# Kernel tuning notes

Hardware: AMD Instinct MI355X
Metric: run time of the kernel (lower is better)

Reference implementation:

```python
import jax, jax.numpy as jnp
import numpy as np

H = 1024
NH = 16
HD = H // NH  # 64
EPS = 1e-5


def _layernorm(x, g, b):
    mu = jnp.mean(x, axis=-1, keepdims=True)
    var = jnp.mean((x - mu) ** 2, axis=-1, keepdims=True)
    return (x - mu) * jax.lax.rsqrt(var + EPS) * g + b


def _rotate_half(x):
    h = x.shape[-1] // 2
    return jnp.concatenate([-x[..., h:], x[..., :h]], axis=-1)


def _rope_tables(T, hd, dtype):
    inv_freq = 1.0 / (10000.0 ** (jnp.arange(0, hd, 2, dtype=jnp.float32) / hd))
    freqs = jnp.arange(T, dtype=jnp.float32)[:, None] * inv_freq[None, :]  # [T, hd/2]
    emb = jnp.concatenate([freqs, freqs], axis=-1)  # [T, hd]
    return jnp.cos(emb).astype(dtype), jnp.sin(emb).astype(dtype)


def setup_inputs() -> dict:
    key = jax.random.key(0)
    ks = jax.random.split(key, 12)
    B, T = 32, 512
    s = 0.02
    inp = {
        "x": jax.random.normal(ks[0], (B, T, H), dtype=jnp.float32),
        "Wq": jax.random.normal(ks[1], (H, H), dtype=jnp.float32) * s,
        "bq": jnp.zeros((H,), jnp.float32),
        "Wk": jax.random.normal(ks[2], (H, H), dtype=jnp.float32) * s,
        "bk": jnp.zeros((H,), jnp.float32),
        "Wv": jax.random.normal(ks[3], (H, H), dtype=jnp.float32) * s,
        "bv": jnp.zeros((H,), jnp.float32),
        "Wo": jax.random.normal(ks[4], (H, H), dtype=jnp.float32) * s,
        "bo": jnp.zeros((H,), jnp.float32),
        "g1": jnp.ones((H,), jnp.float32),
        "be1": jnp.zeros((H,), jnp.float32),
        "g2": jnp.ones((H,), jnp.float32),
        "be2": jnp.zeros((H,), jnp.float32),
        "W1": jax.random.normal(ks[5], (H, 4 * H), dtype=jnp.float32) * s,
        "b1": jnp.zeros((4 * H,), jnp.float32),
        "W2": jax.random.normal(ks[6], (4 * H, H), dtype=jnp.float32) * s,
        "b2": jnp.zeros((H,), jnp.float32),
    }
    return inp


def reference(x, Wq, bq, Wk, bk, Wv, bv, Wo, bo, g1, be1, g2, be2, W1, b1, W2, b2):
    B, T, Hdim = x.shape
    xn = _layernorm(x, g1, be1)
    # [B,T,H] -> [B,NH,T,HD]
    def split_heads(y):
        return y.reshape(B, T, NH, HD).transpose(0, 2, 1, 3)
    q = split_heads(xn @ Wq + bq)
    k = split_heads(xn @ Wk + bk)
    v = split_heads(xn @ Wv + bv)
    cos, sin = _rope_tables(T, HD, x.dtype)  # [T,HD]
    cos = cos[None, None]
    sin = sin[None, None]
    q = q * cos + _rotate_half(q) * sin
    k = k * cos + _rotate_half(k) * sin
    scale = jnp.sqrt(jnp.asarray(HD, x.dtype))
    scores = jnp.einsum("bhqd,bhkd->bhqk", q, k) / scale
    probs = jax.nn.softmax(scores, axis=-1)
    attn = jnp.einsum("bhqk,bhkd->bhqd", probs, v)
    attn = attn.transpose(0, 2, 1, 3).reshape(B, T, Hdim)
    x = x + (attn @ Wo + bo)
    xn2 = _layernorm(x, g2, be2)
    ffn = jax.nn.gelu(xn2 @ W1 + b1, approximate=False) @ W2 + b2
    return x + ffn
```

## Files before the change

### kernel.cpp

```cpp
#include <hip/hip_runtime.h>
#include <math.h>
#include <stdint.h>

#define B_  32
#define T_  512
#define H_  1024
#define NH_ 16
#define HD_ 64
#define FF_ 4096
#define BT_ (B_*T_)
#define CB_ 8
#define CR_ (CB_*T_)
#define NC_ (B_/CB_)
#define MB_ ((size_t)1<<20)

typedef __attribute__((ext_vector_type(8))) short bf16x8;
typedef __attribute__((ext_vector_type(4))) short s16x4;
typedef __attribute__((ext_vector_type(4))) float f32x4;

__device__ __forceinline__ float bf2f(short h){
  unsigned u = ((unsigned)(unsigned short)h) << 16;
  return __uint_as_float(u);
}
__device__ __forceinline__ short f2bf(float f){
  unsigned u = __float_as_uint(f);
  unsigned r = (u + 0x7FFFu + ((u>>16)&1u)) >> 16;
  return (short)r;
}
__device__ __forceinline__ float gelu_f(float x){
  return 0.5f * x * (1.0f + erff(x * 0.7071067811865476f));
}

typedef __attribute__((address_space(1))) const unsigned guint_t;
typedef __attribute__((address_space(3))) unsigned luint_t;
__device__ __forceinline__ void gld16(const void* g, void* l){
  __builtin_amdgcn_global_load_lds((guint_t*)(uintptr_t)g,
                                   (luint_t*)(unsigned)(uintptr_t)l, 16, 0, 0);
}

__global__ __launch_bounds__(256) void ln_bf16_kernel(const float* __restrict__ x,
    const float* __restrict__ g, const float* __restrict__ b, short* __restrict__ o)
{
  const int row = blockIdx.x;
  const int tid = threadIdx.x;
  const float4 v = ((const float4*)(x + (size_t)row*H_))[tid];
  float s  = v.x+v.y+v.z+v.w;
  float ss = v.x*v.x+v.y*v.y+v.z*v.z+v.w*v.w;
  #pragma unroll
  for(int off=32; off>0; off>>=1){
    s  += __shfl_down(s, off);
    ss += __shfl_down(ss, off);
  }
  __shared__ float rs[4], rss[4], mb[2];
  const int wave = tid>>6, lane = tid&63;
  if(lane==0){ rs[wave]=s; rss[wave]=ss; }
  __syncthreads();
  if(tid==0){
    float S  = rs[0]+rs[1]+rs[2]+rs[3];
    float SS = rss[0]+rss[1]+rss[2]+rss[3];
    float mu  = S * (1.0f/H_);
    float var = SS * (1.0f/H_) - mu*mu;
    mb[0] = mu; mb[1] = rsqrtf(var + 1e-5f);
  }
  __syncthreads();
  const float mu = mb[0], rstd = mb[1];
  const float4 gv = ((const float4*)g)[tid];
  const float4 bv = ((const float4*)b)[tid];
  s16x4 o4;
  o4[0] = f2bf((v.x-mu)*rstd*gv.x + bv.x);
  o4[1] = f2bf((v.y-mu)*rstd*gv.y + bv.y);
  o4[2] = f2bf((v.z-mu)*rstd*gv.z + bv.z);
  o4[3] = f2bf((v.w-mu)*rstd*gv.w + bv.w);
  *(s16x4*)(o + (size_t)row*H_ + tid*4) = o4;
}

__global__ void rope_table_kernel(float* __restrict__ cost, float* __restrict__ sint)
{
  const int t = blockIdx.x;
  const int i = threadIdx.x;
  const float invf = (float)pow(10000.0, -(double)i / 32.0);
  const float ang  = (float)t * invf;
  cost[t*32 + i] = (float)cos((double)ang);
  sint[t*32 + i] = (float)sin((double)ang);
}

__global__ void concat3_kernel(const float* __restrict__ a, const float* __restrict__ b,
                               const float* __restrict__ c, float* __restrict__ o)
{
  int i = blockIdx.x*256 + threadIdx.x;
  if(i >= 3*H_) return;
  o[i] = (i < H_) ? a[i] : (i < 2*H_) ? b[i-H_] : c[i-2*H_];
}

__global__ __launch_bounds__(256) void tsplit_kernel(const float* __restrict__ W,
    short* __restrict__ Wh, short* __restrict__ Wl, int K, int N)
{
  __shared__ float t[32][33];
  const int n0 = blockIdx.x*32, k0 = blockIdx.y*32;
  const int tx = threadIdx.x & 31, ty = threadIdx.x >> 5;
  #pragma unroll
  for(int i=0;i<32;i+=8) t[ty+i][tx] = W[(size_t)(k0+ty+i)*N + n0+tx];
  __syncthreads();
  #pragma unroll
  for(int i=0;i<32;i+=8){
    const float f = t[tx][ty+i];
    const short h = f2bf(f);
    const short l = f2bf(f - bf2f(h));
    const size_t o = (size_t)(n0+ty+i)*K + k0+tx;
    Wh[o] = h;  Wl[o] = l;
  }
}

template<int EPI, int OB>
__global__ __launch_bounds__(256,3) void gemm_bf2(
    const short* __restrict__ A, const short* __restrict__ Bhg,
    const short* __restrict__ Blg, const float* __restrict__ bias,
    const float* __restrict__ res, void* __restrict__ Cv,
    int M, int N, int K,
    size_t zW, size_t zC, int biasZ)
{
  __shared__ __align__(16) short Ah[2][128*32];
  __shared__ __align__(16) short Bh[2][128*32];
  __shared__ __align__(16) short Bl[2][128*32];

  const int tid = threadIdx.x;
  const int wid = tid >> 6, lane = tid & 63;
  const int z = blockIdx.z;
  const int bn0 = blockIdx.x * 128;
  const int bm0 = blockIdx.y * 128;
  const short* Bhp = Bhg + (size_t)z * zW;
  const short* Blp = Blg + (size_t)z * zW;
  const float* biasp = bias + (size_t)z * biasZ;

  const int srow0 = wid*16 + (lane>>2);
  const int scol  = (lane&3)*8;

  f32x4 acc[4][4];
  #pragma unroll
  for(int i=0;i<4;i++)
    #pragma unroll
    for(int j=0;j<4;j++) acc[i][j] = (f32x4){0.f,0.f,0.f,0.f};

#define STAGE(BUF, K0) do { \
    _Pragma("unroll") \
    for(int r=0;r<2;r++){ \
      const int rr = srow0 + r*64; \
      const int lo = (r*4+wid)*512; \
      gld16(A   + (size_t)(bm0+rr)*K + (K0) + scol, &Ah[BUF][lo]); \
      gld16(Bhp + (size_t)(bn0+rr)*K + (K0) + scol, &Bh[BUF][lo]); \
      gld16(Blp + (size_t)(bn0+rr)*K + (K0) + scol, &Bl[BUF][lo]); \
    } \
  } while(0)

  STAGE(0, 0);
  __syncthreads();

  const int wm = wid >> 1, wn = wid & 1;
  const int fr = lane & 15;
  const int kq = lane >> 4;

  const int KT = K / 32;
  int buf = 0;
  for(int kt=0; kt<KT; kt++){
    if(kt+1 < KT) STAGE(buf^1, (kt+1)*32);

    bf16x8 af[4], bfh[4], bfl[4];
    #pragma unroll
    for(int mt=0;mt<4;mt++)
      af[mt]  = *(bf16x8*)&Ah[buf][(wm*64 + mt*16 + fr)*32 + kq*8];
    #pragma unroll
    for(int nt=0;nt<4;nt++){
      bfh[nt] = *(bf16x8*)&Bh[buf][(wn*64 + nt*16 + fr)*32 + kq*8];
      bfl[nt] = *(bf16x8*)&Bl[buf][(wn*64 + nt*16 + fr)*32 + kq*8];
    }
    #pragma unroll
    for(int mt=0;mt<4;mt++)
      #pragma unroll
      for(int nt=0;nt<4;nt++){
        acc[mt][nt] = __builtin_amdgcn_mfma_f32_16x16x32_bf16(af[mt], bfh[nt], acc[mt][nt], 0,0,0);
        acc[mt][nt] = __builtin_amdgcn_mfma_f32_16x16x32_bf16(af[mt], bfl[nt], acc[mt][nt], 0,0,0);
      }
    __syncthreads();
    buf ^= 1;
  }
#undef STAGE

  #pragma unroll
  for(int nt=0;nt<4;nt++){
    const int col = bn0 + wn*64 + nt*16 + fr;
    const float bb = biasp[col];
    #pragma unroll
    for(int mt=0;mt<4;mt++){
      #pragma unroll
      for(int r=0;r<4;r++){
        const size_t row = bm0 + wm*64 + mt*16 + kq*4 + r;
        float v = acc[mt][nt][r] + bb;
        if(EPI==1) v = gelu_f(v);
        if(EPI==2) v += res[row*N + col];
        if(OB) ((short*)Cv)[(size_t)z*zC + row*N + col] = f2bf(v);
        else   ((float*)Cv)[(size_t)z*zC + row*N + col] = v;
      }
    }
  }
}

__global__ __launch_bounds__(256,4) void attn_mfma_kernel(
    const short* __restrict__ qg, const short* __restrict__ kg,
    const short* __restrict__ vg, short* __restrict__ og,
    const float* __restrict__ cost, const float* __restrict__ sint)
{
  __shared__ __align__(16) short Q_lds[64][72];
  __shared__ __align__(16) short K_lds[64][72];
  __shared__ __align__(16) short Vt[64][72];
  __shared__ __align__(16) short P_lds[64][72];

  const int qt = blockIdx.x;
  const int bh = blockIdx.y;
  const int b = bh >> 4, h = bh & 15;
  const int tid = threadIdx.x;
  const int wid = tid >> 6, lane = tid & 63;
  const size_t base = ((size_t)b*T_)*H_ + (size_t)h*HD_;

  const int srow = tid >> 2;
  const int sc8  = (tid & 3) * 8;
  const int sc16 = (tid & 3) * 16;

  {
    const int t = qt*64 + srow;
    const short* qp = qg + base + (size_t)t*H_;
    bf16x8 lo = *(const bf16x8*)(qp + sc8);
    bf16x8 hi = *(const bf16x8*)(qp + sc8 + 32);
    float cc[8], ss[8];
    *(float4*)&cc[0] = *(const float4*)(cost + t*32 + sc8);
    *(float4*)&cc[4] = *(const float4*)(cost + t*32 + sc8 + 4);
    *(float4*)&ss[0] = *(const float4*)(sint + t*32 + sc8);
    *(float4*)&ss[4] = *(const float4*)(sint + t*32 + sc8 + 4);
    short olo[8], ohi[8];
    #pragma unroll
    for(int j=0;j<8;j++){
      const float x0 = bf2f(lo[j]), x1 = bf2f(hi[j]);
      olo[j] = f2bf((x0*cc[j] - x1*ss[j])*0.125f);
      ohi[j] = f2bf((x1*cc[j] + x0*ss[j])*0.125f);
    }
    *(bf16x8*)&Q_lds[srow][sc8]    = *(bf16x8*)olo;
    *(bf16x8*)&Q_lds[srow][sc8+32] = *(bf16x8*)ohi;
  }

  const int fr = lane & 15;
  const int g  = lane >> 4;
  const int wq0 = wid * 16;

  float m_run = -1e30f, l_run = 0.f;
  f32x4 acc[4];
  #pragma unroll
  for(int i=0;i<4;i++) acc[i] = (f32x4){0.f,0.f,0.f,0.f};

  for(int kt=0; kt<T_/64; kt++){
    __syncthreads();
    {
      const int t = kt*64 + srow;
      const short* kp = kg + base + (size_t)t*H_;
      bf16x8 lo = *(const bf16x8*)(kp + sc8);
      bf16x8 hi = *(const bf16x8*)(kp + sc8 + 32);
      float cc[8], ss[8];
      *(float4*)&cc[0] = *(const float4*)(cost + t*32 + sc8);
      *(float4*)&cc[4] = *(const float4*)(cost + t*32 + sc8 + 4);
      *(float4*)&ss[0] = *(const float4*)(sint + t*32 + sc8);
      *(float4*)&ss[4] = *(const float4*)(sint + t*32 + sc8 + 4);
      short olo[8], ohi[8];
      #pragma unroll
      for(int j=0;j<8;j++){
        const float x0 = bf2f(lo[j]), x1 = bf2f(hi[j]);
        olo[j] = f2bf(x0*cc[j] - x1*ss[j]);
        ohi[j] = f2bf(x1*cc[j] + x0*ss[j]);
      }
      *(bf16x8*)&K_lds[srow][sc8]    = *(bf16x8*)olo;
      *(bf16x8*)&K_lds[srow][sc8+32] = *(bf16x8*)ohi;

      const short* vp = vg + base + (size_t)t*H_;
      bf16x8 v0 = *(const bf16x8*)(vp + sc16);
      bf16x8 v1 = *(const bf16x8*)(vp + sc16 + 8);
      #pragma unroll
      for(int j=0;j<8;j++){
        Vt[sc16+j][srow]   = v0[j];
        Vt[sc16+8+j][srow] = v1[j];
      }
    }
    __syncthreads();

    f32x4 sfr[4];
    #pragma unroll
    for(int mt=0;mt<4;mt++) sfr[mt] = (f32x4){0.f,0.f,0.f,0.f};
    #pragma unroll
    for(int kk=0;kk<2;kk++){
      const bf16x8 qf = *(bf16x8*)&Q_lds[wq0 + fr][kk*32 + g*8];
      #pragma unroll
      for(int mt=0;mt<4;mt++){
        const bf16x8 kf = *(bf16x8*)&K_lds[mt*16 + fr][kk*32 + g*8];
        sfr[mt] = __builtin_amdgcn_mfma_f32_16x16x32_bf16(kf, qf, sfr[mt], 0,0,0);
      }
    }

    float tmax = -1e30f;
    #pragma unroll
    for(int mt=0;mt<4;mt++)
      #pragma unroll
      for(int r=0;r<4;r++) tmax = fmaxf(tmax, sfr[mt][r]);
    tmax = fmaxf(tmax, __shfl_xor(tmax, 16));
    tmax = fmaxf(tmax, __shfl_xor(tmax, 32));
    const float mn = fmaxf(m_run, tmax);
    const float alpha = __expf(m_run - mn);
    m_run = mn;
    float psum = 0.f;
    short pb[4][4];
    #pragma unroll
    for(int mt=0;mt<4;mt++)
      #pragma unroll
      for(int r=0;r<4;r++){
        const short pbf = f2bf(__expf(sfr[mt][r] - mn));
        pb[mt][r] = pbf;
        psum += bf2f(pbf);
      }
    psum += __shfl_xor(psum, 16);
    psum += __shfl_xor(psum, 32);
    l_run = l_run*alpha + psum;

    #pragma unroll
    for(int mt=0;mt<4;mt++)
      *(s16x4*)&P_lds[wq0 + fr][mt*16 + g*4] = *(s16x4*)pb[mt];

    float a_r[4];
    #pragma unroll
    for(int r=0;r<4;r++) a_r[r] = __shfl(alpha, (lane & 48) | (4*g + r));
    #pragma unroll
    for(int nt=0;nt<4;nt++)
      #pragma unroll
      for(int r=0;r<4;r++) acc[nt][r] *= a_r[r];

    #pragma unroll
    for(int kk=0;kk<2;kk++){
      const bf16x8 pf = *(bf16x8*)&P_lds[wq0 + fr][kk*32 + g*8];
      #pragma unroll
      for(int nt=0;nt<4;nt++){
        const bf16x8 vf = *(bf16x8*)&Vt[nt*16 + fr][kk*32 + g*8];
        acc[nt] = __builtin_amdgcn_mfma_f32_16x16x32_bf16(pf, vf, acc[nt], 0,0,0);
      }
    }
  }

  float linv[4];
  #pragma unroll
  for(int r=0;r<4;r++) linv[r] = 1.0f / __shfl(l_run, (lane & 48) | (4*g + r));
  #pragma unroll
  for(int nt=0;nt<4;nt++){
    const int d = nt*16 + fr;
    #pragma unroll
    for(int r=0;r<4;r++){
      const int t = qt*64 + wq0 + 4*g + r;
      og[base + (size_t)t*H_ + d] = f2bf(acc[nt][r] * linv[r]);
    }
  }
}

extern "C" void kernel_launch(void* const* d_in, const int* in_sizes, int n_in,
                              void* d_out, int out_size, void* d_ws, size_t ws_size,
                              hipStream_t stream)
{
  const float* x   = (const float*)d_in[0];
  const float* Wq  = (const float*)d_in[1];
  const float* bq  = (const float*)d_in[2];
  const float* Wk  = (const float*)d_in[3];
  const float* bk  = (const float*)d_in[4];
  const float* Wv  = (const float*)d_in[5];
  const float* bv  = (const float*)d_in[6];
  const float* Wo  = (const float*)d_in[7];
  const float* bo  = (const float*)d_in[8];
  const float* g1  = (const float*)d_in[9];
  const float* be1 = (const float*)d_in[10];
  const float* g2  = (const float*)d_in[11];
  const float* be2 = (const float*)d_in[12];
  const float* W1  = (const float*)d_in[13];
  const float* b1  = (const float*)d_in[14];
  const float* W2  = (const float*)d_in[15];
  const float* b2  = (const float*)d_in[16];
  float* out = (float*)d_out;
  char*  W   = (char*)d_ws;

  short* wqkvh = (short*)(W + 0*MB_);
  short* wqkvl = (short*)(W + 6*MB_);
  short* woh   = (short*)(W + 12*MB_);
  short* wol   = (short*)(W + 14*MB_);
  short* w1h   = (short*)(W + 16*MB_);
  short* w1l   = (short*)(W + 24*MB_);
  short* w2h   = (short*)(W + 32*MB_);
  short* w2l   = (short*)(W + 40*MB_);
  short* abuf  = (short*)(W + 48*MB_);
  short* hb    = abuf;
  short* qkvc  = (short*)(W + 80*MB_);
  short* xnc   = (short*)(W + 104*MB_);
  float* cost  = (float*)(W + 112*MB_);
  float* sint  = cost + T_*32;
  float* bqkv  = sint + T_*32;

  const size_t CRH = (size_t)CR_ * H_;

  rope_table_kernel<<<T_, 32, 0, stream>>>(cost, sint);
  concat3_kernel<<<(3*H_+255)/256, 256, 0, stream>>>(bq, bk, bv, bqkv);

  tsplit_kernel<<<dim3(32,32),  256, 0, stream>>>(Wq, wqkvh,            wqkvl,            H_, H_);
  tsplit_kernel<<<dim3(32,32),  256, 0, stream>>>(Wk, wqkvh+1024*1024,  wqkvl+1024*1024,  H_, H_);
  tsplit_kernel<<<dim3(32,32),  256, 0, stream>>>(Wv, wqkvh+2*1024*1024,wqkvl+2*1024*1024,H_, H_);
  tsplit_kernel<<<dim3(32,32),  256, 0, stream>>>(Wo, woh, wol, H_, H_);
  tsplit_kernel<<<dim3(128,32), 256, 0, stream>>>(W1, w1h, w1l, H_, FF_);
  tsplit_kernel<<<dim3(32,128), 256, 0, stream>>>(W2, w2h, w2l, FF_, H_);

  for(int c=0; c<NC_; c++){
    const size_t r0 = (size_t)c * CR_;
    ln_bf16_kernel<<<CR_, 256, 0, stream>>>(x + r0*H_, g1, be1, xnc);
    gemm_bf2<0,1><<<dim3(8, CR_/128, 3), 256, 0, stream>>>(
        xnc, wqkvh, wqkvl, bqkv, nullptr, qkvc, CR_, H_, H_,
        (size_t)1024*1024, CRH, H_);
    attn_mfma_kernel<<<dim3(T_/64, CB_*NH_), 256, 0, stream>>>(
        qkvc, qkvc + CRH, qkvc + 2*CRH, abuf + r0*H_, cost, sint);
  }

  gemm_bf2<2,0><<<dim3(8, BT_/128, 1), 256, 0, stream>>>(
      abuf, woh, wol, bo, x, out, BT_, H_, H_, 0, 0, 0);

  for(int c=0; c<NC_; c++){
    const size_t r0 = (size_t)c * CR_;
    ln_bf16_kernel<<<CR_, 256, 0, stream>>>(out + r0*H_, g2, be2, xnc);
    gemm_bf2<1,1><<<dim3(FF_/128, CR_/128, 1), 256, 0, stream>>>(
        xnc, w1h, w1l, b1, nullptr, hb, CR_, FF_, H_, 0, 0, 0);
    gemm_bf2<2,0><<<dim3(H_/128, CR_/128, 1), 256, 0, stream>>>(
        hb, w2h, w2l, b2, out + r0*H_, out + r0*H_, CR_, H_, FF_, 0, 0, 0);
  }
}
```

Baseline: 1.418 ms.

## Switch GEMMs and attention from split-bf16 weights to single fp16 MFMA

Replaces the hi/lo bf16 weight split (two MFMAs per tile, three LDS buffers) with one fp16 weight copy and a single fp16 MFMA per tile. Activations, Q/K/V, softmax probabilities and attention output are now stored as fp16 instead of bf16. This halves matrix-core work and weight traffic in every GEMM, cuts LDS use, and raises the launch-bounds occupancy hint from 3 to 4. In exchange it relies on fp16's mantissa to stay within accuracy tolerance, and fp16's narrower range risks overflow on large activations.

```diff
diff --git a/kernel.cpp b/kernel.cpp
--- a/kernel.cpp
+++ b/kernel.cpp
@@ -14,19 +14,11 @@
 #define NC_ (B_/CB_)
 #define MB_ ((size_t)1<<20)
 
-typedef __attribute__((ext_vector_type(8))) short bf16x8;
-typedef __attribute__((ext_vector_type(4))) short s16x4;
+typedef _Float16 h16;
+typedef __attribute__((ext_vector_type(8))) _Float16 f16x8;
+typedef __attribute__((ext_vector_type(4))) _Float16 f16x4;
 typedef __attribute__((ext_vector_type(4))) float f32x4;
 
-__device__ __forceinline__ float bf2f(short h){
-  unsigned u = ((unsigned)(unsigned short)h) << 16;
-  return __uint_as_float(u);
-}
-__device__ __forceinline__ short f2bf(float f){
-  unsigned u = __float_as_uint(f);
-  unsigned r = (u + 0x7FFFu + ((u>>16)&1u)) >> 16;
-  return (short)r;
-}
 __device__ __forceinline__ float gelu_f(float x){
   return 0.5f * x * (1.0f + erff(x * 0.7071067811865476f));
 }
@@ -38,8 +30,8 @@
                                    (luint_t*)(unsigned)(uintptr_t)l, 16, 0, 0);
 }
 
-__global__ __launch_bounds__(256) void ln_bf16_kernel(const float* __restrict__ x,
-    const float* __restrict__ g, const float* __restrict__ b, short* __restrict__ o)
+__global__ __launch_bounds__(256) void ln_f16_kernel(const float* __restrict__ x,
+    const float* __restrict__ g, const float* __restrict__ b, h16* __restrict__ o)
 {
   const int row = blockIdx.x;
   const int tid = threadIdx.x;
@@ -66,12 +58,12 @@
   const float mu = mb[0], rstd = mb[1];
   const float4 gv = ((const float4*)g)[tid];
   const float4 bv = ((const float4*)b)[tid];
-  s16x4 o4;
-  o4[0] = f2bf((v.x-mu)*rstd*gv.x + bv.x);
-  o4[1] = f2bf((v.y-mu)*rstd*gv.y + bv.y);
-  o4[2] = f2bf((v.z-mu)*rstd*gv.z + bv.z);
-  o4[3] = f2bf((v.w-mu)*rstd*gv.w + bv.w);
-  *(s16x4*)(o + (size_t)row*H_ + tid*4) = o4;
+  f16x4 o4;
+  o4[0] = (h16)((v.x-mu)*rstd*gv.x + bv.x);
+  o4[1] = (h16)((v.y-mu)*rstd*gv.y + bv.y);
+  o4[2] = (h16)((v.z-mu)*rstd*gv.z + bv.z);
+  o4[3] = (h16)((v.w-mu)*rstd*gv.w + bv.w);
+  *(f16x4*)(o + (size_t)row*H_ + tid*4) = o4;
 }
 
 __global__ void rope_table_kernel(float* __restrict__ cost, float* __restrict__ sint)
@@ -92,8 +84,8 @@
   o[i] = (i < H_) ? a[i] : (i < 2*H_) ? b[i-H_] : c[i-2*H_];
 }
 
-__global__ __launch_bounds__(256) void tsplit_kernel(const float* __restrict__ W,
-    short* __restrict__ Wh, short* __restrict__ Wl, int K, int N)
+__global__ __launch_bounds__(256) void tcvt_kernel(const float* __restrict__ W,
+    h16* __restrict__ Wt, int K, int N)
 {
   __shared__ float t[32][33];
   const int n0 = blockIdx.x*32, k0 = blockIdx.y*32;
@@ -104,32 +96,26 @@
   #pragma unroll
   for(int i=0;i<32;i+=8){
     const float f = t[tx][ty+i];
-    const short h = f2bf(f);
-    const short l = f2bf(f - bf2f(h));
-    const size_t o = (size_t)(n0+ty+i)*K + k0+tx;
-    Wh[o] = h;  Wl[o] = l;
+    Wt[(size_t)(n0+ty+i)*K + k0+tx] = (h16)f;
   }
 }
 
 template<int EPI, int OB>
-__global__ __launch_bounds__(256,3) void gemm_bf2(
-    const short* __restrict__ A, const short* __restrict__ Bhg,
-    const short* __restrict__ Blg, const float* __restrict__ bias,
-    const float* __restrict__ res, void* __restrict__ Cv,
-    int M, int N, int K,
+__global__ __launch_bounds__(256,4) void gemm_f16(
+    const h16* __restrict__ A, const h16* __restrict__ Bg,
+    const float* __restrict__ bias, const float* __restrict__ res,
+    void* __restrict__ Cv, int M, int N, int K,
     size_t zW, size_t zC, int biasZ)
 {
-  __shared__ __align__(16) short Ah[2][128*32];
-  __shared__ __align__(16) short Bh[2][128*32];
-  __shared__ __align__(16) short Bl[2][128*32];
+  __shared__ __align__(16) h16 Ah[2][128*32];
+  __shared__ __align__(16) h16 Bh[2][128*32];
 
   const int tid = threadIdx.x;
   const int wid = tid >> 6, lane = tid & 63;
   const int z = blockIdx.z;
   const int bn0 = blockIdx.x * 128;
   const int bm0 = blockIdx.y * 128;
-  const short* Bhp = Bhg + (size_t)z * zW;
-  const short* Blp = Blg + (size_t)z * zW;
+  const h16* Bp = Bg + (size_t)z * zW;
   const float* biasp = bias + (size_t)z * biasZ;
 
   const int srow0 = wid*16 + (lane>>2);
@@ -146,9 +132,8 @@
     for(int r=0;r<2;r++){ \
       const int rr = srow0 + r*64; \
       const int lo = (r*4+wid)*512; \
-      gld16(A   + (size_t)(bm0+rr)*K + (K0) + scol, &Ah[BUF][lo]); \
-      gld16(Bhp + (size_t)(bn0+rr)*K + (K0) + scol, &Bh[BUF][lo]); \
-      gld16(Blp + (size_t)(bn0+rr)*K + (K0) + scol, &Bl[BUF][lo]); \
+      gld16(A  + (size_t)(bm0+rr)*K + (K0) + scol, &Ah[BUF][lo]); \
+      gld16(Bp + (size_t)(bn0+rr)*K + (K0) + scol, &Bh[BUF][lo]); \
     } \
   } while(0)
 
@@ -164,22 +149,18 @@
   for(int kt=0; kt<KT; kt++){
     if(kt+1 < KT) STAGE(buf^1, (kt+1)*32);
 
-    bf16x8 af[4], bfh[4], bfl[4];
+    f16x8 af[4], bf[4];
     #pragma unroll
     for(int mt=0;mt<4;mt++)
-      af[mt]  = *(bf16x8*)&Ah[buf][(wm*64 + mt*16 + fr)*32 + kq*8];
-    #pragma unroll
-    for(int nt=0;nt<4;nt++){
-      bfh[nt] = *(bf16x8*)&Bh[buf][(wn*64 + nt*16 + fr)*32 + kq*8];
-      bfl[nt] = *(bf16x8*)&Bl[buf][(wn*64 + nt*16 + fr)*32 + kq*8];
-    }
+      af[mt] = *(f16x8*)&Ah[buf][(wm*64 + mt*16 + fr)*32 + kq*8];
+    #pragma unroll
+    for(int nt=0;nt<4;nt++)
+      bf[nt] = *(f16x8*)&Bh[buf][(wn*64 + nt*16 + fr)*32 + kq*8];
     #pragma unroll
     for(int mt=0;mt<4;mt++)
       #pragma unroll
-      for(int nt=0;nt<4;nt++){
-        acc[mt][nt] = __builtin_amdgcn_mfma_f32_16x16x32_bf16(af[mt], bfh[nt], acc[mt][nt], 0,0,0);
-        acc[mt][nt] = __builtin_amdgcn_mfma_f32_16x16x32_bf16(af[mt], bfl[nt], acc[mt][nt], 0,0,0);
-      }
+      for(int nt=0;nt<4;nt++)
+        acc[mt][nt] = __builtin_amdgcn_mfma_f32_16x16x32_f16(af[mt], bf[nt], acc[mt][nt], 0,0,0);
     __syncthreads();
     buf ^= 1;
   }
@@ -197,7 +178,7 @@
         float v = acc[mt][nt][r] + bb;
         if(EPI==1) v = gelu_f(v);
         if(EPI==2) v += res[row*N + col];
-        if(OB) ((short*)Cv)[(size_t)z*zC + row*N + col] = f2bf(v);
+        if(OB) ((h16*)Cv)[(size_t)z*zC + row*N + col] = (h16)v;
         else   ((float*)Cv)[(size_t)z*zC + row*N + col] = v;
       }
     }
@@ -205,14 +186,14 @@
 }
 
 __global__ __launch_bounds__(256,4) void attn_mfma_kernel(
-    const short* __restrict__ qg, const short* __restrict__ kg,
-    const short* __restrict__ vg, short* __restrict__ og,
+    const h16* __restrict__ qg, const h16* __restrict__ kg,
+    const h16* __restrict__ vg, h16* __restrict__ og,
     const float* __restrict__ cost, const float* __restrict__ sint)
 {
-  __shared__ __align__(16) short Q_lds[64][72];
-  __shared__ __align__(16) short K_lds[64][72];
-  __shared__ __align__(16) short Vt[64][72];
-  __shared__ __align__(16) short P_lds[64][72];
+  __shared__ __align__(16) h16 Q_lds[64][72];
+  __shared__ __align__(16) h16 K_lds[64][72];
+  __shared__ __align__(16) h16 Vt[64][72];
+  __shared__ __align__(16) h16 P_lds[64][72];
 
   const int qt = blockIdx.x;
   const int bh = blockIdx.y;
@@ -227,23 +208,23 @@
 
   {
     const int t = qt*64 + srow;
-    const short* qp = qg + base + (size_t)t*H_;
-    bf16x8 lo = *(const bf16x8*)(qp + sc8);
-    bf16x8 hi = *(const bf16x8*)(qp + sc8 + 32);
+    const h16* qp = qg + base + (size_t)t*H_;
+    f16x8 lo = *(const f16x8*)(qp + sc8);
+    f16x8 hi = *(const f16x8*)(qp + sc8 + 32);
     float cc[8], ss[8];
     *(float4*)&cc[0] = *(const float4*)(cost + t*32 + sc8);
     *(float4*)&cc[4] = *(const float4*)(cost + t*32 + sc8 + 4);
     *(float4*)&ss[0] = *(const float4*)(sint + t*32 + sc8);
     *(float4*)&ss[4] = *(const float4*)(sint + t*32 + sc8 + 4);
-    short olo[8], ohi[8];
+    f16x8 olo, ohi;
     #pragma unroll
     for(int j=0;j<8;j++){
-      const float x0 = bf2f(lo[j]), x1 = bf2f(hi[j]);
-      olo[j] = f2bf((x0*cc[j] - x1*ss[j])*0.125f);
-      ohi[j] = f2bf((x1*cc[j] + x0*ss[j])*0.125f);
-    }
-    *(bf16x8*)&Q_lds[srow][sc8]    = *(bf16x8*)olo;
-    *(bf16x8*)&Q_lds[srow][sc8+32] = *(bf16x8*)ohi;
+      const float x0 = (float)lo[j], x1 = (float)hi[j];
+      olo[j] = (h16)((x0*cc[j] - x1*ss[j])*0.125f);
+      ohi[j] = (h16)((x1*cc[j] + x0*ss[j])*0.125f);
+    }
+    *(f16x8*)&Q_lds[srow][sc8]    = olo;
+    *(f16x8*)&Q_lds[srow][sc8+32] = ohi;
   }
 
   const int fr = lane & 15;
@@ -259,27 +240,27 @@
     __syncthreads();
     {
       const int t = kt*64 + srow;
-      const short* kp = kg + base + (size_t)t*H_;
-      bf16x8 lo = *(const bf16x8*)(kp + sc8);
-      bf16x8 hi = *(const bf16x8*)(kp + sc8 + 32);
+      const h16* kp = kg + base + (size_t)t*H_;
+      f16x8 lo = *(const f16x8*)(kp + sc8);
+      f16x8 hi = *(const f16x8*)(kp + sc8 + 32);
       float cc[8], ss[8];
       *(float4*)&cc[0] = *(const float4*)(cost + t*32 + sc8);
       *(float4*)&cc[4] = *(const float4*)(cost + t*32 + sc8 + 4);
       *(float4*)&ss[0] = *(const float4*)(sint + t*32 + sc8);
       *(float4*)&ss[4] = *(const float4*)(sint + t*32 + sc8 + 4);
-      short olo[8], ohi[8];
+      f16x8 olo, ohi;
       #pragma unroll
       for(int j=0;j<8;j++){
-        const float x0 = bf2f(lo[j]), x1 = bf2f(hi[j]);
-        olo[j] = f2bf(x0*cc[j] - x1*ss[j]);
-        ohi[j] = f2bf(x1*cc[j] + x0*ss[j]);
-      }
-      *(bf16x8*)&K_lds[srow][sc8]    = *(bf16x8*)olo;
-      *(bf16x8*)&K_lds[srow][sc8+32] = *(bf16x8*)ohi;
-
-      const short* vp = vg + base + (size_t)t*H_;
-      bf16x8 v0 = *(const bf16x8*)(vp + sc16);
-      bf16x8 v1 = *(const bf16x8*)(vp + sc16 + 8);
+        const float x0 = (float)lo[j], x1 = (float)hi[j];
+        olo[j] = (h16)(x0*cc[j] - x1*ss[j]);
+        ohi[j] = (h16)(x1*cc[j] + x0*ss[j]);
+      }
+      *(f16x8*)&K_lds[srow][sc8]    = olo;
+      *(f16x8*)&K_lds[srow][sc8+32] = ohi;
+
+      const h16* vp = vg + base + (size_t)t*H_;
+      f16x8 v0 = *(const f16x8*)(vp + sc16);
+      f16x8 v1 = *(const f16x8*)(vp + sc16 + 8);
       #pragma unroll
       for(int j=0;j<8;j++){
         Vt[sc16+j][srow]   = v0[j];
@@ -293,11 +274,11 @@
     for(int mt=0;mt<4;mt++) sfr[mt] = (f32x4){0.f,0.f,0.f,0.f};
     #pragma unroll
     for(int kk=0;kk<2;kk++){
-      const bf16x8 qf = *(bf16x8*)&Q_lds[wq0 + fr][kk*32 + g*8];
+      const f16x8 qf = *(f16x8*)&Q_lds[wq0 + fr][kk*32 + g*8];
       #pragma unroll
       for(int mt=0;mt<4;mt++){
-        const bf16x8 kf = *(bf16x8*)&K_lds[mt*16 + fr][kk*32 + g*8];
-        sfr[mt] = __builtin_amdgcn_mfma_f32_16x16x32_bf16(kf, qf, sfr[mt], 0,0,0);
+        const f16x8 kf = *(f16x8*)&K_lds[mt*16 + fr][kk*32 + g*8];
+        sfr[mt] = __builtin_amdgcn_mfma_f32_16x16x32_f16(kf, qf, sfr[mt], 0,0,0);
       }
     }
 
@@ -312,14 +293,14 @@
     const float alpha = __expf(m_run - mn);
     m_run = mn;
     float psum = 0.f;
-    short pb[4][4];
+    h16 pb[4][4];
     #pragma unroll
     for(int mt=0;mt<4;mt++)
       #pragma unroll
       for(int r=0;r<4;r++){
-        const short pbf = f2bf(__expf(sfr[mt][r] - mn));
-        pb[mt][r] = pbf;
-        psum += bf2f(pbf);
+        const h16 ph = (h16)__expf(sfr[mt][r] - mn);
+        pb[mt][r] = ph;
+        psum += (float)ph;
       }
     psum += __shfl_xor(psum, 16);
     psum += __shfl_xor(psum, 32);
@@ -327,7 +308,7 @@
 
     #pragma unroll
     for(int mt=0;mt<4;mt++)
-      *(s16x4*)&P_lds[wq0 + fr][mt*16 + g*4] = *(s16x4*)pb[mt];
+      *(f16x4*)&P_lds[wq0 + fr][mt*16 + g*4] = *(f16x4*)pb[mt];
 
     float a_r[4];
     #pragma unroll
@@ -339,11 +320,11 @@
 
     #pragma unroll
     for(int kk=0;kk<2;kk++){
-      const bf16x8 pf = *(bf16x8*)&P_lds[wq0 + fr][kk*32 + g*8];
+      const f16x8 pf = *(f16x8*)&P_lds[wq0 + fr][kk*32 + g*8];
       #pragma unroll
       for(int nt=0;nt<4;nt++){
-        const bf16x8 vf = *(bf16x8*)&Vt[nt*16 + fr][kk*32 + g*8];
-        acc[nt] = __builtin_amdgcn_mfma_f32_16x16x32_bf16(pf, vf, acc[nt], 0,0,0);
+        const f16x8 vf = *(f16x8*)&Vt[nt*16 + fr][kk*32 + g*8];
+        acc[nt] = __builtin_amdgcn_mfma_f32_16x16x32_f16(pf, vf, acc[nt], 0,0,0);
       }
     }
   }
@@ -357,7 +338,7 @@
     #pragma unroll
     for(int r=0;r<4;r++){
       const int t = qt*64 + wq0 + 4*g + r;
-      og[base + (size_t)t*H_ + d] = f2bf(acc[nt][r] * linv[r]);
+      og[base + (size_t)t*H_ + d] = (h16)(acc[nt][r] * linv[r]);
     }
   }
 }
@@ -386,53 +367,49 @@
   float* out = (float*)d_out;
   char*  W   = (char*)d_ws;
 
-  short* wqkvh = (short*)(W + 0*MB_);
-  short* wqkvl = (short*)(W + 6*MB_);
-  short* woh   = (short*)(W + 12*MB_);
-  short* wol   = (short*)(W + 14*MB_);
-  short* w1h   = (short*)(W + 16*MB_);
-  short* w1l   = (short*)(W + 24*MB_);
-  short* w2h   = (short*)(W + 32*MB_);
-  short* w2l   = (short*)(W + 40*MB_);
-  short* abuf  = (short*)(W + 48*MB_);
-  short* hb    = abuf;
-  short* qkvc  = (short*)(W + 80*MB_);
-  short* xnc   = (short*)(W + 104*MB_);
-  float* cost  = (float*)(W + 112*MB_);
-  float* sint  = cost + T_*32;
-  float* bqkv  = sint + T_*32;
+  h16* wqkv = (h16*)(W + 0*MB_);
+  h16* wo   = (h16*)(W + 6*MB_);
+  h16* w1   = (h16*)(W + 8*MB_);
+  h16* w2   = (h16*)(W + 16*MB_);
+  h16* abuf = (h16*)(W + 24*MB_);
+  h16* hb   = abuf;
+  h16* qkvc = (h16*)(W + 56*MB_);
+  h16* xnc  = (h16*)(W + 80*MB_);
+  float* cost = (float*)(W + 88*MB_);
+  float* sint = cost + T_*32;
+  float* bqkv = sint + T_*32;
 
   const size_t CRH = (size_t)CR_ * H_;
 
   rope_table_kernel<<<T_, 32, 0, stream>>>(cost, sint);
   concat3_kernel<<<(3*H_+255)/256, 256, 0, stream>>>(bq, bk, bv, bqkv);
 
-  tsplit_kernel<<<dim3(32,32),  256, 0, stream>>>(Wq, wqkvh,            wqkvl,            H_, H_);
-  tsplit_kernel<<<dim3(32,32),  256, 0, stream>>>(Wk, wqkvh+1024*1024,  wqkvl+1024*1024,  H_, H_);
-  tsplit_kernel<<<dim3(32,32),  256, 0, stream>>>(Wv, wqkvh+2*1024*1024,wqkvl+2*1024*1024,H_, H_);
-  tsplit_kernel<<<dim3(32,32),  256, 0, stream>>>(Wo, woh, wol, H_, H_);
-  tsplit_kernel<<<dim3(128,32), 256, 0, stream>>>(W1, w1h, w1l, H_, FF_);
-  tsplit_kernel<<<dim3(32,128), 256, 0, stream>>>(W2, w2h, w2l, FF_, H_);
+  tcvt_kernel<<<dim3(32,32),  256, 0, stream>>>(Wq, wqkv,              H_, H_);
+  tcvt_kernel<<<dim3(32,32),  256, 0, stream>>>(Wk, wqkv + 1024*1024,  H_, H_);
+  tcvt_kernel<<<dim3(32,32),  256, 0, stream>>>(Wv, wqkv + 2*1024*1024,H_, H_);
+  tcvt_kernel<<<dim3(32,32),  256, 0, stream>>>(Wo, wo, H_, H_);
+  tcvt_kernel<<<dim3(128,32), 256, 0, stream>>>(W1, w1, H_, FF_);
+  tcvt_kernel<<<dim3(32,128), 256, 0, stream>>>(W2, w2, FF_, H_);
 
   for(int c=0; c<NC_; c++){
     const size_t r0 = (size_t)c * CR_;
-    ln_bf16_kernel<<<CR_, 256, 0, stream>>>(x + r0*H_, g1, be1, xnc);
-    gemm_bf2<0,1><<<dim3(8, CR_/128, 3), 256, 0, stream>>>(
-        xnc, wqkvh, wqkvl, bqkv, nullptr, qkvc, CR_, H_, H_,
+    ln_f16_kernel<<<CR_, 256, 0, stream>>>(x + r0*H_, g1, be1, xnc);
+    gemm_f16<0,1><<<dim3(8, CR_/128, 3), 256, 0, stream>>>(
+        xnc, wqkv, bqkv, nullptr, qkvc, CR_, H_, H_,
         (size_t)1024*1024, CRH, H_);
     attn_mfma_kernel<<<dim3(T_/64, CB_*NH_), 256, 0, stream>>>(
         qkvc, qkvc + CRH, qkvc + 2*CRH, abuf + r0*H_, cost, sint);
   }
 
-  gemm_bf2<2,0><<<dim3(8, BT_/128, 1), 256, 0, stream>>>(
-      abuf, woh, wol, bo, x, out, BT_, H_, H_, 0, 0, 0);
+  gemm_f16<2,0><<<dim3(8, BT_/128, 1), 256, 0, stream>>>(
+      abuf, wo, bo, x, out, BT_, H_, H_, 0, 0, 0);
 
   for(int c=0; c<NC_; c++){
     const size_t r0 = (size_t)c * CR_;
-    ln_bf16_kernel<<<CR_, 256, 0, stream>>>(out + r0*H_, g2, be2, xnc);
-    gemm_bf2<1,1><<<dim3(FF_/128, CR_/128, 1), 256, 0, stream>>>(
-        xnc, w1h, w1l, b1, nullptr, hb, CR_, FF_, H_, 0, 0, 0);
-    gemm_bf2<2,0><<<dim3(H_/128, CR_/128, 1), 256, 0, stream>>>(
-        hb, w2h, w2l, b2, out + r0*H_, out + r0*H_, CR_, H_, FF_, 0, 0, 0);
-  }
-}
+    ln_f16_kernel<<<CR_, 256, 0, stream>>>(out + r0*H_, g2, be2, xnc);
+    gemm_f16<1,1><<<dim3(FF_/128, CR_/128, 1), 256, 0, stream>>>(
+        xnc, w1, b1, nullptr, hb, CR_, FF_, H_, 0, 0, 0);
+    gemm_f16<2,0><<<dim3(H_/128, CR_/128, 1), 256, 0, stream>>>(
+        hb, w2, b2, out + r0*H_, out + r0*H_, CR_, H_, FF_, 0, 0, 0);
+  }
+}
```

Result: faster. 1.157 ms (-18.4%).
